# Kernel tuning notes

Hardware: AMD Instinct MI355X
Metric: run time of the kernel (lower is better)

The kernel has to match this reference:

```python
import jax, jax.numpy as jnp
import numpy as np

B, T, C, H = 8, 1024, 768, 12
D = C // H  # head dim = 64


def setup_inputs() -> dict:
    key = jax.random.key(0)
    ks = jax.random.split(key, 5)
    x = jax.random.normal(ks[0], (B, T, C), dtype=jnp.float32)
    W_attn = jax.random.normal(ks[1], (C, 3 * C), dtype=jnp.float32) * 0.02
    b_attn = jnp.zeros((3 * C,), dtype=jnp.float32)
    W_proj = jax.random.normal(ks[2], (C, C), dtype=jnp.float32) * 0.02
    b_proj = jnp.zeros((C,), dtype=jnp.float32)
    return {"x": x, "W_attn": W_attn, "b_attn": b_attn, "W_proj": W_proj, "b_proj": b_proj}


def reference(x, W_attn, b_attn, W_proj, b_proj):
    Bx, Tx, Cx = x.shape
    qkv = x @ W_attn + b_attn                      # [B,T,3C]
    q, k, v = jnp.split(qkv, 3, axis=-1)           # each [B,T,C]
    # [B,T,C] -> [B,H,T,D]
    q = q.reshape(Bx, Tx, H, D).transpose(0, 2, 1, 3)
    k = k.reshape(Bx, Tx, H, D).transpose(0, 2, 1, 3)
    v = v.reshape(Bx, Tx, H, D).transpose(0, 2, 1, 3)
    scale = 1.0 / jnp.sqrt(jnp.asarray(D, dtype=x.dtype))
    att = jnp.einsum('bhqd,bhkd->bhqk', q, k) * scale   # [B,H,T,T]
    causal = jnp.tril(jnp.ones((Tx, Tx), dtype=bool))    # [T,T]
    att = jnp.where(causal[None, None, :, :], att, jnp.asarray(-jnp.inf, dtype=att.dtype))
    att = jax.nn.softmax(att, axis=-1)
    y = jnp.einsum('bhqk,bhkd->bhqd', att, v)            # [B,H,T,D]
    y = y.transpose(0, 2, 1, 3).reshape(Bx, Tx, Cx)      # [B,T,C]
    return y @ W_proj + b_proj
```

## Files before the change

kernel.cpp:

```cpp
#include <hip/hip_runtime.h>
#include <stdint.h>

typedef short short8 __attribute__((ext_vector_type(8)));
typedef float f32x4 __attribute__((ext_vector_type(4)));

__device__ __forceinline__ unsigned short f2bf(float f) {
    union { float f; uint32_t u; } v; v.f = f;
    uint32_t u = v.u;
    u += 0x7FFFu + ((u >> 16) & 1u);
    return (unsigned short)(u >> 16);
}

__device__ __forceinline__ void gload_lds16(const void* g, void* l) {
    __builtin_amdgcn_global_load_lds(
        (const __attribute__((address_space(1))) void*)g,
        (__attribute__((address_space(3))) void*)l, 16, 0, 0);
}

__device__ __forceinline__ void transpose_body(const float* __restrict__ in,
                                               unsigned short* __restrict__ out,
                                               int R, int Cc, int bx, int by,
                                               float (*tile)[33]) {
    int c0 = bx * 32, r0 = by * 32;
    int tr = threadIdx.x / 32, c = threadIdx.x % 32;
#pragma unroll
    for (int rr = tr; rr < 32; rr += 8)
        tile[rr][c] = in[(size_t)(r0 + rr) * Cc + c0 + c];
    __syncthreads();
#pragma unroll
    for (int rr = tr; rr < 32; rr += 8)
        out[(size_t)(c0 + rr) * R + r0 + c] = f2bf(tile[c][rr]);
}

__global__ void k_prep(const float* __restrict__ x, unsigned short* __restrict__ xb,
                       const float* __restrict__ Wa, unsigned short* __restrict__ WaT,
                       const float* __restrict__ Wp, unsigned short* __restrict__ WpT) {
    __shared__ float tile[32][33];
    const int blk = blockIdx.x;
    if (blk < 6144) {
        int i = blk * 256 + threadIdx.x;
        float4 f = ((const float4*)x)[i];
        ushort4 o;
        o.x = f2bf(f.x); o.y = f2bf(f.y); o.z = f2bf(f.z); o.w = f2bf(f.w);
        ((ushort4*)xb)[i] = o;
    } else if (blk < 6144 + 1728) {
        int id = blk - 6144;
        transpose_body(Wa, WaT, 768, 2304, id % 72, id / 72, tile);
    } else {
        int id = blk - 7872;
        transpose_body(Wp, WpT, 768, 768, id % 24, id / 24, tile);
    }
}

template<bool F32OUT, bool VSPLIT>
__global__ __launch_bounds__(256, 3)
void k_gemm_bt(const unsigned short* __restrict__ A, const unsigned short* __restrict__ BT,
               const float* __restrict__ bias, void* __restrict__ Cout,
               unsigned short* __restrict__ Vt,
               int M, int N, int K) {
    __shared__ unsigned short As[2][128][32];
    __shared__ unsigned short Bs[2][128][32];
    const int nbx = gridDim.x;
    const int total = nbx * gridDim.y;
    const int id = blockIdx.y * nbx + blockIdx.x;
    const int sw = (id & 7) * (total >> 3) + (id >> 3);
    const int m0 = (sw / nbx) * 128, n0 = (sw % nbx) * 128;
    const int t = threadIdx.x;
    const int w = t >> 6, l = t & 63;
    const int wm = (w >> 1) * 64, wn = (w & 1) * 64;
    const int lr = l & 15, lg = l >> 4;
    const int srow = w * 32 + (l >> 2);
    const int scol = (l & 3) * 8;
    const unsigned short* pa = &A [(size_t)(m0 + srow) * K + scol];
    const unsigned short* pb = &BT[(size_t)(n0 + srow) * K + scol];

    f32x4 acc[4][4];
#pragma unroll
    for (int i = 0; i < 4; ++i)
#pragma unroll
        for (int j = 0; j < 4; ++j)
#pragma unroll
            for (int r = 0; r < 4; ++r) acc[i][j][r] = 0.0f;

    for (int k0 = 0; k0 < K; k0 += 64) {
        __syncthreads();
        gload_lds16(pa + k0,                        &As[0][w * 32][0]);
        gload_lds16(pa + (size_t)16 * K + k0,       &As[0][w * 32 + 16][0]);
        gload_lds16(pa + k0 + 32,                   &As[1][w * 32][0]);
        gload_lds16(pa + (size_t)16 * K + k0 + 32,  &As[1][w * 32 + 16][0]);
        gload_lds16(pb + k0,                        &Bs[0][w * 32][0]);
        gload_lds16(pb + (size_t)16 * K + k0,       &Bs[0][w * 32 + 16][0]);
        gload_lds16(pb + k0 + 32,                   &Bs[1][w * 32][0]);
        gload_lds16(pb + (size_t)16 * K + k0 + 32,  &Bs[1][w * 32 + 16][0]);
        __syncthreads();
#pragma unroll
        for (int p = 0; p < 2; ++p) {
            short8 af[4], bfv[4];
#pragma unroll
            for (int f = 0; f < 4; ++f) {
                af [f] = *(const short8*)&As[p][wm + f * 16 + lr][lg * 8];
                bfv[f] = *(const short8*)&Bs[p][wn + f * 16 + lr][lg * 8];
            }
#pragma unroll
            for (int mf = 0; mf < 4; ++mf)
#pragma unroll
                for (int nf = 0; nf < 4; ++nf)
                    acc[mf][nf] = __builtin_amdgcn_mfma_f32_16x16x32_bf16(af[mf], bfv[nf], acc[mf][nf], 0, 0, 0);
        }
    }

#pragma unroll
    for (int mf = 0; mf < 4; ++mf)
#pragma unroll
        for (int nf = 0; nf < 4; ++nf) {
            int n = n0 + wn + nf * 16 + lr;
            int mbase = m0 + wm + mf * 16 + lg * 4;
            float bv = bias[n];
            if (VSPLIT && n >= 1536) {
                int hh = (n - 1536) >> 6, dd = (n - 1536) & 63;
                int bb = mbase >> 10, tt = mbase & 1023;
                ushort4 o;
                o.x = f2bf(acc[mf][nf][0] + bv);
                o.y = f2bf(acc[mf][nf][1] + bv);
                o.z = f2bf(acc[mf][nf][2] + bv);
                o.w = f2bf(acc[mf][nf][3] + bv);
                *(ushort4*)&Vt[(((size_t)bb * 12 + hh) * 64 + dd) * 1024 + tt] = o;
            } else {
#pragma unroll
                for (int r = 0; r < 4; ++r) {
                    float v = acc[mf][nf][r] + bv;
                    if (F32OUT) ((float*)Cout)[(size_t)(mbase + r) * N + n] = v;
                    else ((unsigned short*)Cout)[(size_t)(mbase + r) * N + n] = f2bf(v);
                }
            }
        }
}

__global__ __launch_bounds__(256, 3)
void k_attn(const unsigned short* __restrict__ qkv, const unsigned short* __restrict__ vt,
            unsigned short* __restrict__ y) {
    __shared__ unsigned short Ks[2][64][80];
    __shared__ unsigned short Vs[2][64][80];
    __shared__ unsigned short Ps[4][16][72];
    const int p = blockIdx.x;
    const int v = (p & 7) * 96 + (p >> 3);
    const int bh = v >> 3;
    const int qt = 7 - (v & 7);
    const int b = bh / 12, h = bh % 12;
    const int t = threadIdx.x, w = t >> 6, l = t & 63, lr = l & 15, lg = l >> 4;
    const int q0 = qt * 128;

    const unsigned short* qbase = qkv + (size_t)b * 1024 * 2304 + h * 64;
    const unsigned short* kbase = qbase + 768;
    const unsigned short* vbase = vt + (size_t)bh * 64 * 1024;

    const int srow = t >> 2, scol = (t & 3) * 8;
    const unsigned short* kst = &kbase[(size_t)srow * 2304 + scol];
    const unsigned short* vst = &vbase[(size_t)srow * 1024 + scol];

    short8 qf[2][2];
#pragma unroll
    for (int g = 0; g < 2; ++g) {
        const unsigned short* qrow = &qbase[(size_t)(q0 + g * 64 + w * 16 + lr) * 2304];
        qf[g][0] = *(const short8*)&qrow[lg * 8];
        qf[g][1] = *(const short8*)&qrow[32 + lg * 8];
    }

    float l_lane[2][4];
    f32x4 o_acc[2][4];
#pragma unroll
    for (int g = 0; g < 2; ++g)
#pragma unroll
        for (int r = 0; r < 4; ++r) {
            l_lane[g][r] = 0.0f;
#pragma unroll
            for (int df = 0; df < 4; ++df) o_acc[g][df][r] = 0.0f;
        }

    {
        uint4 ka = *(const uint4*)(kst);
        uint4 kb = *(const uint4*)(kst + 32);
        uint4 va = *(const uint4*)(vst);
        uint4 vb = *(const uint4*)(vst + 32);
        *(uint4*)&Ks[0][srow][scol]      = ka;
        *(uint4*)&Ks[0][srow][scol + 32] = kb;
        *(uint4*)&Vs[0][srow][scol]      = va;
        *(uint4*)&Vs[0][srow][scol + 32] = vb;
    }
    __syncthreads();

    const int nkt = qt * 2 + 2;
    int cur = 0;
    for (int kti = 0; kti < nkt; ++kti) {
        const int kt = kti * 64;
        const bool more = (kti + 1 < nkt);
        uint4 nka, nkb, nva, nvb;
        if (more) {
            const int kn = kt + 64;
            nka = *(const uint4*)(kst + (size_t)kn * 2304);
            nkb = *(const uint4*)(kst + (size_t)kn * 2304 + 32);
            nva = *(const uint4*)(vst + kn);
            nvb = *(const uint4*)(vst + kn + 32);
        }

#pragma unroll
        for (int g = 0; g < 2; ++g) {
            if (g == 0 && kti == nkt - 1) continue;
            const bool diag = (kti == nkt - 2 + g);
            const int qw0 = q0 + g * 64 + w * 16;

            f32x4 s[4];
            __builtin_amdgcn_s_setprio(1);
#pragma unroll
            for (int nf = 0; nf < 4; ++nf) {
                f32x4 z;
#pragma unroll
                for (int r = 0; r < 4; ++r) z[r] = 0.0f;
                if (!diag || nf <= w) {
                    short8 kf0 = *(const short8*)&Ks[cur][nf * 16 + lr][lg * 8];
                    short8 kf1 = *(const short8*)&Ks[cur][nf * 16 + lr][32 + lg * 8];
                    z = __builtin_amdgcn_mfma_f32_16x16x32_bf16(qf[g][0], kf0, z, 0, 0, 0);
                    z = __builtin_amdgcn_mfma_f32_16x16x32_bf16(qf[g][1], kf1, z, 0, 0, 0);
                }
                s[nf] = z;
            }
            __builtin_amdgcn_s_setprio(0);
            float pv[4][4];
#pragma unroll
            for (int nf = 0; nf < 4; ++nf) {
                int col = kt + nf * 16 + lr;
#pragma unroll
                for (int r = 0; r < 4; ++r) {
                    bool ok = !diag || (nf < w) || (col <= qw0 + lg * 4 + r);
                    float e = ok ? __expf(s[nf][r] * 0.125f - 8.0f) : 0.0f;
                    pv[nf][r] = e;
                    l_lane[g][r] += e;
                }
            }
#pragma unroll
            for (int nf = 0; nf < 4; ++nf)
#pragma unroll
                for (int r = 0; r < 4; ++r)
                    Ps[w][lg * 4 + r][nf * 16 + lr] = f2bf(pv[nf][r]);
            short8 pf0 = *(const short8*)&Ps[w][lr][lg * 8];
            short8 pf1 = *(const short8*)&Ps[w][lr][32 + lg * 8];
            __builtin_amdgcn_s_setprio(1);
#pragma unroll
            for (int df = 0; df < 4; ++df) {
                short8 vf0 = *(const short8*)&Vs[cur][df * 16 + lr][lg * 8];
                short8 vf1 = *(const short8*)&Vs[cur][df * 16 + lr][32 + lg * 8];
                o_acc[g][df] = __builtin_amdgcn_mfma_f32_16x16x32_bf16(pf0, vf0, o_acc[g][df], 0, 0, 0);
                o_acc[g][df] = __builtin_amdgcn_mfma_f32_16x16x32_bf16(pf1, vf1, o_acc[g][df], 0, 0, 0);
            }
            __builtin_amdgcn_s_setprio(0);
        }

        if (more) {
            *(uint4*)&Ks[cur ^ 1][srow][scol]      = nka;
            *(uint4*)&Ks[cur ^ 1][srow][scol + 32] = nkb;
            *(uint4*)&Vs[cur ^ 1][srow][scol]      = nva;
            *(uint4*)&Vs[cur ^ 1][srow][scol + 32] = nvb;
        }
        __syncthreads();
        cur ^= 1;
    }

#pragma unroll
    for (int g = 0; g < 2; ++g)
#pragma unroll
        for (int r = 0; r < 4; ++r) {
            float s_ = l_lane[g][r];
#pragma unroll
            for (int d = 1; d < 16; d <<= 1) s_ += __shfl_xor(s_, d);
            float inv = 1.0f / s_;
            int row = q0 + g * 64 + w * 16 + lg * 4 + r;
#pragma unroll
            for (int df = 0; df < 4; ++df)
                y[((size_t)b * 1024 + row) * 768 + h * 64 + df * 16 + lr] = f2bf(o_acc[g][df][r] * inv);
        }
}

extern "C" void kernel_launch(void* const* d_in, const int* in_sizes, int n_in,
                              void* d_out, int out_size, void* d_ws, size_t ws_size,
                              hipStream_t stream) {
    const float* x  = (const float*)d_in[0];
    const float* Wa = (const float*)d_in[1];
    const float* ba = (const float*)d_in[2];
    const float* Wp = (const float*)d_in[3];
    const float* bp = (const float*)d_in[4];
    float* out = (float*)d_out;

    char* ws = (char*)d_ws;
    unsigned short* qkv = (unsigned short*)ws;
    unsigned short* xb  = (unsigned short*)(ws + 37748736);
    unsigned short* WaT = (unsigned short*)(ws + 37748736 + 12582912);
    unsigned short* WpT = (unsigned short*)(ws + 37748736 + 12582912 + 3538944);
    unsigned short* y   = xb;
    unsigned short* vtb = (unsigned short*)d_out;

    k_prep<<<8448, 256, 0, stream>>>(x, xb, Wa, WaT, Wp, WpT);
    k_gemm_bt<false, true><<<dim3(18, 64), 256, 0, stream>>>(xb, WaT, ba, qkv, vtb, 8192, 2304, 768);
    k_attn<<<768, 256, 0, stream>>>(qkv, vtb, y);
    k_gemm_bt<true, false><<<dim3(6, 64), 256, 0, stream>>>(y, WpT, bp, out, nullptr, 8192, 768, 768);
}
```

Measured before the change: 119.2 us.

## Triple-buffer GEMM LDS staging with async prefetch two steps ahead

Replaces the synchronous two-barrier load-then-compute loop in the bf16 GEMM with a 3-stage LDS ring buffer. Global-to-LDS loads for step k+2 are issued after the MFMAs of step k. Partial vmcnt waits plus a single barrier per 32-wide K step let memory latency overlap with MFMA work. This raises LDS per block to 48KB, which may limit occupancy, and relies on hand-placed waitcnt counts being correct.

```diff
diff --git a/kernel.cpp b/kernel.cpp
--- a/kernel.cpp
+++ b/kernel.cpp
@@ -58,8 +58,8 @@
                const float* __restrict__ bias, void* __restrict__ Cout,
                unsigned short* __restrict__ Vt,
                int M, int N, int K) {
-    __shared__ unsigned short As[2][128][32];
-    __shared__ unsigned short Bs[2][128][32];
+    __shared__ unsigned short As[3][128][32];
+    __shared__ unsigned short Bs[3][128][32];
     const int nbx = gridDim.x;
     const int total = nbx * gridDim.y;
     const int id = blockIdx.y * nbx + blockIdx.x;
@@ -82,32 +82,38 @@
 #pragma unroll
             for (int r = 0; r < 4; ++r) acc[i][j][r] = 0.0f;
 
-    for (int k0 = 0; k0 < K; k0 += 64) {
-        __syncthreads();
-        gload_lds16(pa + k0,                        &As[0][w * 32][0]);
-        gload_lds16(pa + (size_t)16 * K + k0,       &As[0][w * 32 + 16][0]);
-        gload_lds16(pa + k0 + 32,                   &As[1][w * 32][0]);
-        gload_lds16(pa + (size_t)16 * K + k0 + 32,  &As[1][w * 32 + 16][0]);
-        gload_lds16(pb + k0,                        &Bs[0][w * 32][0]);
-        gload_lds16(pb + (size_t)16 * K + k0,       &Bs[0][w * 32 + 16][0]);
-        gload_lds16(pb + k0 + 32,                   &Bs[1][w * 32][0]);
-        gload_lds16(pb + (size_t)16 * K + k0 + 32,  &Bs[1][w * 32 + 16][0]);
-        __syncthreads();
-#pragma unroll
-        for (int p = 0; p < 2; ++p) {
-            short8 af[4], bfv[4];
-#pragma unroll
-            for (int f = 0; f < 4; ++f) {
-                af [f] = *(const short8*)&As[p][wm + f * 16 + lr][lg * 8];
-                bfv[f] = *(const short8*)&Bs[p][wn + f * 16 + lr][lg * 8];
-            }
-#pragma unroll
-            for (int mf = 0; mf < 4; ++mf)
-#pragma unroll
-                for (int nf = 0; nf < 4; ++nf)
-                    acc[mf][nf] = __builtin_amdgcn_mfma_f32_16x16x32_bf16(af[mf], bfv[nf], acc[mf][nf], 0, 0, 0);
-        }
-    }
+    #define STAGE(s_, k_)  do {                                          \
+        gload_lds16(pa + (k_),                  &As[s_][w * 32][0]);     \
+        gload_lds16(pa + (size_t)16 * K + (k_), &As[s_][w * 32 + 16][0]);\
+        gload_lds16(pb + (k_),                  &Bs[s_][w * 32][0]);     \
+        gload_lds16(pb + (size_t)16 * K + (k_), &Bs[s_][w * 32 + 16][0]);\
+    } while (0)
+
+    const int nsteps = K >> 5;
+    STAGE(0, 0);
+    STAGE(1, 32);
+
+#pragma unroll 3
+    for (int k = 0; k < nsteps; ++k) {
+        if (k + 1 < nsteps) asm volatile("s_waitcnt vmcnt(4)" ::: "memory");
+        else                asm volatile("s_waitcnt vmcnt(0)" ::: "memory");
+        __builtin_amdgcn_s_barrier();
+        __builtin_amdgcn_sched_barrier(0);
+        const int s = k % 3;
+        short8 af[4], bfv[4];
+#pragma unroll
+        for (int f = 0; f < 4; ++f) {
+            af [f] = *(const short8*)&As[s][wm + f * 16 + lr][lg * 8];
+            bfv[f] = *(const short8*)&Bs[s][wn + f * 16 + lr][lg * 8];
+        }
+#pragma unroll
+        for (int mf = 0; mf < 4; ++mf)
+#pragma unroll
+            for (int nf = 0; nf < 4; ++nf)
+                acc[mf][nf] = __builtin_amdgcn_mfma_f32_16x16x32_bf16(af[mf], bfv[nf], acc[mf][nf], 0, 0, 0);
+        if (k + 2 < nsteps) STAGE((k + 2) % 3, (k + 2) * 32);
+    }
+    #undef STAGE
 
 #pragma unroll
     for (int mf = 0; mf < 4; ++mf)
```

New measurement: 121.5 us. No clear change (+1.9%).

## Transpose QK^T MFMA operands so P writes are packed, share K fragments across groups

Applied to the files above, without the earlier changes.

The S=QK^T MFMA now takes K as the A operand and Q as B, so each lane holds four consecutive key columns for one query row. That lets P be packed with v_cvt_pk_bf16_f32 into a single 8-byte LDS store per fragment instead of 16 scalar stores. K fragments are loaded once per tile and reused for both query groups. The row-sum reduction shrinks to two cross-lane shuffles plus one broadcast. This cuts LDS traffic and VALU work in the softmax stage, at the cost of more live registers from holding both s0 and s1.

```diff
diff --git a/kernel.cpp b/kernel.cpp
--- a/kernel.cpp
+++ b/kernel.cpp
@@ -9,6 +9,12 @@
     uint32_t u = v.u;
     u += 0x7FFFu + ((u >> 16) & 1u);
     return (unsigned short)(u >> 16);
+}
+
+__device__ __forceinline__ uint32_t cvtpk(float lo, float hi) {
+    uint32_t r;
+    asm("v_cvt_pk_bf16_f32 %0, %1, %2" : "=v"(r) : "v"(lo), "v"(hi));
+    return r;
 }
 
 __device__ __forceinline__ void gload_lds16(const void* g, void* l) {
@@ -166,16 +172,14 @@
         qf[g][1] = *(const short8*)&qrow[32 + lg * 8];
     }
 
-    float l_lane[2][4];
+    float l_loc[2] = {0.0f, 0.0f};
     f32x4 o_acc[2][4];
 #pragma unroll
     for (int g = 0; g < 2; ++g)
 #pragma unroll
-        for (int r = 0; r < 4; ++r) {
-            l_lane[g][r] = 0.0f;
-#pragma unroll
-            for (int df = 0; df < 4; ++df) o_acc[g][df][r] = 0.0f;
-        }
+        for (int df = 0; df < 4; ++df)
+#pragma unroll
+            for (int r = 0; r < 4; ++r) o_acc[g][df][r] = 0.0f;
 
     {
         uint4 ka = *(const uint4*)(kst);
@@ -203,45 +207,54 @@
             nvb = *(const uint4*)(vst + kn + 32);
         }
 
+        const bool act0 = (kti < nkt - 1);
+        const bool dg0  = (kti == nkt - 2);
+        const bool dg1  = (kti == nkt - 1);
+
+        f32x4 s0[4], s1[4];
+        __builtin_amdgcn_s_setprio(1);
+#pragma unroll
+        for (int nf = 0; nf < 4; ++nf) {
+            short8 kf0 = *(const short8*)&Ks[cur][nf * 16 + lr][lg * 8];
+            short8 kf1 = *(const short8*)&Ks[cur][nf * 16 + lr][32 + lg * 8];
+            f32x4 z0, z1;
+#pragma unroll
+            for (int r = 0; r < 4; ++r) { z0[r] = 0.0f; z1[r] = 0.0f; }
+            if (act0 && (!dg0 || nf <= w)) {
+                z0 = __builtin_amdgcn_mfma_f32_16x16x32_bf16(kf0, qf[0][0], z0, 0, 0, 0);
+                z0 = __builtin_amdgcn_mfma_f32_16x16x32_bf16(kf1, qf[0][1], z0, 0, 0, 0);
+            }
+            if (!dg1 || nf <= w) {
+                z1 = __builtin_amdgcn_mfma_f32_16x16x32_bf16(kf0, qf[1][0], z1, 0, 0, 0);
+                z1 = __builtin_amdgcn_mfma_f32_16x16x32_bf16(kf1, qf[1][1], z1, 0, 0, 0);
+            }
+            s0[nf] = z0; s1[nf] = z1;
+        }
+        __builtin_amdgcn_s_setprio(0);
+
 #pragma unroll
         for (int g = 0; g < 2; ++g) {
-            if (g == 0 && kti == nkt - 1) continue;
-            const bool diag = (kti == nkt - 2 + g);
-            const int qw0 = q0 + g * 64 + w * 16;
-
-            f32x4 s[4];
-            __builtin_amdgcn_s_setprio(1);
+            if (g == 0 && !act0) continue;
+            const bool diag = g ? dg1 : dg0;
+            const int row = q0 + g * 64 + w * 16 + lr;
+            float lsum = 0.0f;
 #pragma unroll
             for (int nf = 0; nf < 4; ++nf) {
-                f32x4 z;
-#pragma unroll
-                for (int r = 0; r < 4; ++r) z[r] = 0.0f;
-                if (!diag || nf <= w) {
-                    short8 kf0 = *(const short8*)&Ks[cur][nf * 16 + lr][lg * 8];
-                    short8 kf1 = *(const short8*)&Ks[cur][nf * 16 + lr][32 + lg * 8];
-                    z = __builtin_amdgcn_mfma_f32_16x16x32_bf16(qf[g][0], kf0, z, 0, 0, 0);
-                    z = __builtin_amdgcn_mfma_f32_16x16x32_bf16(qf[g][1], kf1, z, 0, 0, 0);
+                float e[4];
+#pragma unroll
+                for (int r = 0; r < 4; ++r) {
+                    int col = kt + nf * 16 + lg * 4 + r;
+                    bool ok = !diag || (nf < w) || (col <= row);
+                    float sv = g ? s1[nf][r] : s0[nf][r];
+                    e[r] = ok ? __expf(sv * 0.125f - 8.0f) : 0.0f;
+                    lsum += e[r];
                 }
-                s[nf] = z;
-            }
-            __builtin_amdgcn_s_setprio(0);
-            float pv[4][4];
-#pragma unroll
-            for (int nf = 0; nf < 4; ++nf) {
-                int col = kt + nf * 16 + lr;
-#pragma unroll
-                for (int r = 0; r < 4; ++r) {
-                    bool ok = !diag || (nf < w) || (col <= qw0 + lg * 4 + r);
-                    float e = ok ? __expf(s[nf][r] * 0.125f - 8.0f) : 0.0f;
-                    pv[nf][r] = e;
-                    l_lane[g][r] += e;
-                }
-            }
-#pragma unroll
-            for (int nf = 0; nf < 4; ++nf)
-#pragma unroll
-                for (int r = 0; r < 4; ++r)
-                    Ps[w][lg * 4 + r][nf * 16 + lr] = f2bf(pv[nf][r]);
+                uint2 u;
+                u.x = cvtpk(e[0], e[1]);
+                u.y = cvtpk(e[2], e[3]);
+                *(uint2*)&Ps[w][lr][nf * 16 + lg * 4] = u;
+            }
+            l_loc[g] += lsum;
             short8 pf0 = *(const short8*)&Ps[w][lr][lg * 8];
             short8 pf1 = *(const short8*)&Ps[w][lr][32 + lg * 8];
             __builtin_amdgcn_s_setprio(1);
@@ -266,18 +279,19 @@
     }
 
 #pragma unroll
-    for (int g = 0; g < 2; ++g)
+    for (int g = 0; g < 2; ++g) {
+        float dsum = l_loc[g];
+        dsum += __shfl_xor(dsum, 16);
+        dsum += __shfl_xor(dsum, 32);
 #pragma unroll
         for (int r = 0; r < 4; ++r) {
-            float s_ = l_lane[g][r];
-#pragma unroll
-            for (int d = 1; d < 16; d <<= 1) s_ += __shfl_xor(s_, d);
-            float inv = 1.0f / s_;
-            int row = q0 + g * 64 + w * 16 + lg * 4 + r;
+            float inv = 1.0f / __shfl(dsum, lg * 4 + r);
+            int rowy = q0 + g * 64 + w * 16 + lg * 4 + r;
 #pragma unroll
             for (int df = 0; df < 4; ++df)
-                y[((size_t)b * 1024 + row) * 768 + h * 64 + df * 16 + lr] = f2bf(o_acc[g][df][r] * inv);
-        }
+                y[((size_t)b * 1024 + rowy) * 768 + h * 64 + df * 16 + lr] = f2bf(o_acc[g][df][r] * inv);
+        }
+    }
 }
 
 extern "C" void kernel_launch(void* const* d_in, const int* in_sizes, int n_in,
```

Result: faster. 113.8 us (-4.5%).
